# Kernel optimization log

Hardware: AMD Instinct MI355X
Metric: run time of the kernel (lower is better)

Reference implementation:

```python
import jax, jax.numpy as jnp
import numpy as np
import math

D_MODEL = 256
SIGMA = 1.0


def _sinusoidal_pe(L, d_model, dtype=jnp.float32):
    # pe[l, 2i] = sin(l * w_i), pe[l, 2i+1] = cos(l * w_i)
    position = jnp.arange(L, dtype=dtype)[:, None]                       # [L,1]
    div_term = jnp.exp(jnp.arange(0, d_model, 2, dtype=dtype) * (-math.log(10000.0) / d_model))
    pe = jnp.zeros((L, d_model), dtype=dtype)
    pe = pe.at[:, 0::2].set(jnp.sin(position * div_term))
    pe = pe.at[:, 1::2].set(jnp.cos(position * div_term))
    return pe  # [L, d_model]


def setup_inputs() -> dict:
    key = jax.random.key(0)
    # scale 0.05 keeps pairwise sq-distances O(1) so S = exp(-d/2) is non-degenerate
    x = jax.random.normal(key, (4, 4096, 256), dtype=jnp.float32) * 0.05
    return {"x": x}


def reference(x):
    B, L, D = x.shape
    pe = _sinusoidal_pe(L, D_MODEL, dtype=x.dtype)[None]                 # [1,L,D]
    # pairwise squared distances via the expansion ||a||^2+||b||^2-2ab (avoids [B,L,L,D])
    sq = jnp.sum(x * x, axis=-1)                                         # [B,L]
    gram = jnp.einsum('bld,bmd->blm', x, x)                              # [B,L,L]
    dist_sq = jnp.maximum(sq[:, :, None] + sq[:, None, :] - 2.0 * gram, 0.0)
    S = jnp.exp(-dist_sq / (2.0 * SIGMA ** 2))                           # [B,L,L]
    sem = jnp.einsum('blm,bmd->bld', S, x) / jnp.sum(S, axis=-1, keepdims=True)
    return x + pe + sem
```

## Files before the change

kernel.cpp:

```cpp
#include <hip/hip_runtime.h>

typedef unsigned char u8;
typedef float f32x4 __attribute__((ext_vector_type(4)));
typedef float f32x16 __attribute__((ext_vector_type(16)));
typedef int i32x8 __attribute__((ext_vector_type(8)));

#define LL 4096
#define PSTR 144
#define SCALE 16.0f
#define GSCALE (1.0f/256.0f)
#define FREQC (-0.03597789207803197f)
#define ONE_SC 0x7F7F7F7F
#define VBSTR 1048576l

__device__ __forceinline__ i32x8 PK16(uint4 a, uint4 b) {
  i32x8 r;
  r[0] = (int)a.x; r[1] = (int)a.y; r[2] = (int)a.z; r[3] = (int)a.w;
  r[4] = (int)b.x; r[5] = (int)b.y; r[6] = (int)b.z; r[7] = (int)b.w;
  return r;
}

typedef __attribute__((address_space(3))) u8 lds_u8;
typedef __attribute__((address_space(1))) u8 glb_u8;
__device__ __forceinline__ void dma16(const u8* g, u8* l) {
  __builtin_amdgcn_global_load_lds((const glb_u8*)g, (lds_u8*)l, 16, 0, 0);
}

__global__ __launch_bounds__(512) void prep4(const float* __restrict__ x, u8* __restrict__ xbf,
                                             u8* __restrict__ xT, float* __restrict__ sq) {
  __shared__ u8 T2[256 * 80];
  const int blk = blockIdx.x;
  const int b = blk >> 6, ch = blk & 63;
  const int j0 = ch << 6;
  const int tid = threadIdx.x;
  const int wv = tid >> 6, ln = tid & 63;
  const long bL = (long)b * LL;
  const float4* x4 = (const float4*)x + (bL + j0) * 64;
  unsigned* xb4 = (unsigned*)xbf + (bL + j0) * 64;

  #pragma unroll
  for (int g = 0; g < 2; ++g) {
    int pkw[4];
    #pragma unroll
    for (int ii = 0; ii < 4; ++ii) {
      const int row = 8 * wv + 4 * g + ii;
      float4 v = x4[row * 64 + ln];
      float s = v.x * v.x + v.y * v.y + v.z * v.z + v.w * v.w;
      #pragma unroll
      for (int o = 32; o; o >>= 1) s += __shfl_xor(s, o);
      if (ln == 0) sq[bL + j0 + row] = s;
      int pk = __builtin_amdgcn_cvt_pk_fp8_f32(v.x * SCALE, v.y * SCALE, 0, false);
      pk = __builtin_amdgcn_cvt_pk_fp8_f32(v.z * SCALE, v.w * SCALE, pk, true);
      const int sdw = ((((ln >> 2) ^ ((j0 + row) & 15)) << 2)) | (ln & 3);
      xb4[row * 64 + sdw] = (unsigned)pk;
      pkw[ii] = pk;
    }
    const int rb = 8 * wv + 4 * g;
    #pragma unroll
    for (int k = 0; k < 4; ++k) {
      const unsigned sel = (unsigned)(k | ((4 + k) << 8));
      unsigned m01 = __builtin_amdgcn_perm((unsigned)pkw[1], (unsigned)pkw[0], sel);
      unsigned m23 = __builtin_amdgcn_perm((unsigned)pkw[3], (unsigned)pkw[2], sel);
      unsigned tw  = __builtin_amdgcn_perm(m23, m01, 0x05040100u);
      *(unsigned*)(T2 + (4 * ln + k) * 80 + rb) = tw;
    }
  }
  __syncthreads();
  #pragma unroll
  for (int db = 0; db < 2; ++db) {
    const int d = db * 128 + (tid >> 2);
    const int cl = tid & 3;
    const int c16 = ((ch & 1) << 2) | cl;
    const int p = c16 ^ (d & 7);
    uint4 ov = *(const uint4*)(T2 + d * 80 + 16 * cl);
    *(uint4*)(xT + (long)b * VBSTR + (ch >> 1) * 32768 + d * 128 + (p << 4)) = ov;
  }
}

__global__ __launch_bounds__(512, 2) void tpe_main(
    const u8* __restrict__ xbf, const u8* __restrict__ xT,
    const float* __restrict__ sqv,
    const float* __restrict__ x, float* __restrict__ out) {
  __shared__ __align__(16) u8 Kt[2][32768];
  __shared__ __align__(16) u8 Vt[2][32768];
  __shared__ __align__(16) u8 Ps[2][64 * PSTR];
  __shared__ float lred[8][64];
  __shared__ float linv[64];

  const int tid = threadIdx.x;
  const int w = tid >> 6;
  const int lane = tid & 63;
  const int l15 = lane & 15, l31 = lane & 31;
  const int q4 = lane >> 4;
  const int q2 = lane >> 5;

  const int blk = blockIdx.x;
  const int b = (blk & 7) >> 1;
  const int qt = ((blk >> 3) << 1) | (blk & 1);
  const int q0 = qt << 6;
  const long bL = (long)b * LL;

  i32x8 qmx[4][2];
  float qa[4];
  #pragma unroll
  for (int t = 0; t < 4; ++t) {
    const int row = q0 + 16 * t + l15;
    const u8* qrow = xbf + ((bL + row) << 8);
    #pragma unroll
    for (int u = 0; u < 2; ++u) {
      const int cb = 8 * u + 2 * q4;
      uint4 lo = *(const uint4*)(qrow + (((cb + 0) ^ l15) << 4));
      uint4 hi = *(const uint4*)(qrow + (((cb + 1) ^ l15) << 4));
      qmx[t][u] = PK16(lo, hi);
    }
    qa[t] = -0.5f * sqv[bL + row];
  }

  f32x16 oacc[2];
  #pragma unroll
  for (int rb = 0; rb < 2; ++rb)
    #pragma unroll
    for (int k = 0; k < 16; ++k) oacc[rb][k] = 0.f;
  float rsacc[4] = {0.f, 0.f, 0.f, 0.f};

  const u8* kbat = xbf + (bL << 8);
  const u8* vbat = xT + (long)b * VBSTR;
  const int vrow = (32 * w + l31) << 7;
  const int vk7 = l31 & 7;

  i32x8 vfA[2], vfB[2];

  #pragma unroll
  for (int c = 0; c < 4; ++c) {
    int off = c * 8192 + tid * 16;
    dma16(kbat + off, Kt[0] + off);
    dma16(vbat + off, Vt[0] + off);
  }
  __syncthreads();

#define TPE_ITER(IT, KCUR, KNXT, VCUR, VNXT, PPREV, PCUR, VFC, VFN)                         \
  {                                                                                         \
    const int j0 = (IT) << 7;                                                               \
    if ((IT) < 31) {  \
      const u8* ks = kbat + ((long)((IT) + 1) << 15);                                       \
      const u8* vs = vbat + ((long)((IT) + 1) << 15);                                       \
      _Pragma("unroll")                                                                     \
      for (int c = 0; c < 4; ++c) {                                                         \
        int off = c * 8192 + tid * 16;                                                      \
        dma16(ks + off, (KNXT) + off);                                                      \
        dma16(vs + off, (VNXT) + off);                                                      \
      }                                                                                     \
    }                                                                                       \
    float4 skv4 = *(const float4*)(sqv + bL + j0 + 16 * w + 4 * q4);                        \
    if ((IT) != 0) {  \
      _Pragma("unroll")                                                                     \
      for (int u = 0; u < 2; ++u) {                                                         \
        const u8* pr0 = (PPREV) + l31 * PSTR + 64 * u + 32 * q2;                            \
        i32x8 pa0 = PK16(*(const uint4*)(pr0), *(const uint4*)(pr0 + 16));                  \
        i32x8 pa1 = PK16(*(const uint4*)(pr0 + 32 * PSTR),                                  \
                         *(const uint4*)(pr0 + 32 * PSTR + 16));                            \
        oacc[0] = __builtin_amdgcn_mfma_scale_f32_32x32x64_f8f6f4(                          \
            pa0, VFC[u], oacc[0], 0, 0, 0, ONE_SC, 0, ONE_SC);                              \
        oacc[1] = __builtin_amdgcn_mfma_scale_f32_32x32x64_f8f6f4(                          \
            pa1, VFC[u], oacc[1], 0, 0, 0, ONE_SC, 0, ONE_SC);                              \
      }                                                                                     \
    }                                                                                       \
    _Pragma("unroll")           \
    for (int u = 0; u < 2; ++u) {                                                           \
      const int cb = 4 * u + 2 * q2;                                                        \
      uint4 v0 = *(const uint4*)((VCUR) + vrow + (((cb + 0) ^ vk7) << 4));                  \
      uint4 v1 = *(const uint4*)((VCUR) + vrow + (((cb + 1) ^ vk7) << 4));                  \
      VFN[u] = PK16(v0, v1);                                                                \
    }                                                                                       \
    {                            \
      const int krow = 16 * w + l15;                                                        \
      const u8* kb2 = (KCUR) + krow * 256;                                                  \
      f32x4 sacc[4];                                                                        \
      _Pragma("unroll")                                                                     \
      for (int t = 0; t < 4; ++t) {                                                         \
        sacc[t][0] = 0.f; sacc[t][1] = 0.f; sacc[t][2] = 0.f; sacc[t][3] = 0.f;             \
      }                                                                                     \
      _Pragma("unroll")                                                                     \
      for (int u = 0; u < 2; ++u) {                                                         \
        const int cb = 8 * u + 2 * q4;                                                      \
        uint4 klo = *(const uint4*)(kb2 + (((cb + 0) ^ l15) << 4));                         \
        uint4 khi = *(const uint4*)(kb2 + (((cb + 1) ^ l15) << 4));                         \
        i32x8 af = PK16(klo, khi);                                                          \
        _Pragma("unroll")                                                                   \
        for (int t = 0; t < 4; ++t)                                                         \
          sacc[t] = __builtin_amdgcn_mfma_scale_f32_16x16x128_f8f6f4(                       \
              af, qmx[t][u], sacc[t], 0, 0, 0, ONE_SC, 0, ONE_SC);                          \
      }                                                                                     \
      _Pragma("unroll")        \
      for (int t = 0; t < 4; ++t) {                 \
        float p0 = __expf(fminf(fmaf(sacc[t][0], GSCALE, qa[t] + skv4.x), 0.f));            \
        float p1 = __expf(fminf(fmaf(sacc[t][1], GSCALE, qa[t] + skv4.y), 0.f));            \
        float p2 = __expf(fminf(fmaf(sacc[t][2], GSCALE, qa[t] + skv4.z), 0.f));            \
        float p3 = __expf(fminf(fmaf(sacc[t][3], GSCALE, qa[t] + skv4.w), 0.f));            \
        rsacc[t] += (p0 + p1) + (p2 + p3);                                                  \
        int pk = __builtin_amdgcn_cvt_pk_fp8_f32(p0, p1, 0, false);                         \
        pk = __builtin_amdgcn_cvt_pk_fp8_f32(p2, p3, pk, true);                             \
        *(int*)((PCUR) + (16 * t + l15) * PSTR + 16 * w + 4 * q4) = pk;                     \
      }                                                                                     \
    }                                                                                       \
    __syncthreads();                \
  }

  for (int it2 = 0; it2 < 16; ++it2) {
    TPE_ITER(2 * it2,     Kt[0], Kt[1], Vt[0], Vt[1], Ps[1], Ps[0], vfA, vfB)
    TPE_ITER(2 * it2 + 1, Kt[1], Kt[0], Vt[1], Vt[0], Ps[0], Ps[1], vfB, vfA)
  }
#undef TPE_ITER

  #pragma unroll
  for (int u = 0; u < 2; ++u) {
    const u8* pr0 = Ps[1] + l31 * PSTR + 64 * u + 32 * q2;
    i32x8 pa0 = PK16(*(const uint4*)(pr0), *(const uint4*)(pr0 + 16));
    i32x8 pa1 = PK16(*(const uint4*)(pr0 + 32 * PSTR), *(const uint4*)(pr0 + 32 * PSTR + 16));
    oacc[0] = __builtin_amdgcn_mfma_scale_f32_32x32x64_f8f6f4(
        pa0, vfA[u], oacc[0], 0, 0, 0, ONE_SC, 0, ONE_SC);
    oacc[1] = __builtin_amdgcn_mfma_scale_f32_32x32x64_f8f6f4(
        pa1, vfA[u], oacc[1], 0, 0, 0, ONE_SC, 0, ONE_SC);
  }

  #pragma unroll
  for (int t = 0; t < 4; ++t) {
    float r = rsacc[t];
    r += __shfl_xor(r, 16);
    r += __shfl_xor(r, 32);
    if (lane < 16) lred[w][16 * t + l15] = r;
  }
  __syncthreads();
  if (tid < 64) {
    float s = 0.f;
    #pragma unroll
    for (int ww = 0; ww < 8; ++ww) s += lred[ww][tid];
    linv[tid] = 0.0625f / s;
  }
  __syncthreads();
  const int col = 32 * w + l31;
  const float freq = __expf((float)(col & ~1) * FREQC);
  #pragma unroll
  for (int rb = 0; rb < 2; ++rb) {
    #pragma unroll
    for (int reg = 0; reg < 16; ++reg) {
      int row = 32 * rb + 4 * q2 + (reg & 3) + 8 * (reg >> 2);
      int l = q0 + row;
      float ang = (float)l * freq;
      float pv = (col & 1) ? __cosf(ang) : __sinf(ang);
      long off = ((bL + l) << 8) + col;
      out[off] = oacc[rb][reg] * linv[row] + x[off] + pv;
    }
  }
}

extern "C" void kernel_launch(void* const* d_in, const int* in_sizes, int n_in,
                              void* d_out, int out_size, void* d_ws, size_t ws_size,
                              hipStream_t stream) {
  const float* x = (const float*)d_in[0];
  float* out = (float*)d_out;
  char* ws = (char*)d_ws;
  u8* xbf = (u8*)ws;
  u8* xT = (u8*)(ws + 4194304);
  float* sq = (float*)(ws + 8388608);
  prep4<<<256, 512, 0, stream>>>(x, xbf, xT, sq);
  tpe_main<<<256, 512, 0, stream>>>(xbf, xT, sq, x, out);
}
```

Before: 123.7 us.

## Swizzle fp8 K/V at 32-byte granularity and fold log2e into exp2

Changes the XOR swizzle of the fp8 K (xbf) and transposed V (xT) buffers from 16-byte to 32-byte chunks, so each MFMA operand fragment becomes a single 32-byte LDS/global load instead of two 16-byte loads packed together. It also pre-multiplies the squared norms and gram scale by log2(e) so the Gaussian kernel uses exp2f directly. The aim is fewer LDS read instructions and a cheaper exponential. The coarser swizzle may raise LDS bank conflicts, and the new layout must match between the prep kernel and the main kernel.

Result: slower. 133.9 us (+8.3%).

```diff
diff --git a/kernel.cpp b/kernel.cpp
--- a/kernel.cpp
+++ b/kernel.cpp
@@ -9,6 +9,8 @@
 #define PSTR 144
 #define SCALE 16.0f
 #define GSCALE (1.0f/256.0f)
+#define L2E 1.44269504f
+#define GS2 (1.44269504f/256.0f)
 #define FREQC (-0.03597789207803197f)
 #define ONE_SC 0x7F7F7F7F
 #define VBSTR 1048576l
@@ -26,7 +28,7 @@
   __builtin_amdgcn_global_load_lds((const glb_u8*)g, (lds_u8*)l, 16, 0, 0);
 }
 
-__global__ __launch_bounds__(512) void prep4(const float* __restrict__ x, u8* __restrict__ xbf,
+__global__ __launch_bounds__(512) void prep5(const float* __restrict__ x, u8* __restrict__ xbf,
                                              u8* __restrict__ xT, float* __restrict__ sq) {
   __shared__ u8 T2[256 * 80];
   const int blk = blockIdx.x;
@@ -51,7 +53,7 @@
       if (ln == 0) sq[bL + j0 + row] = s;
       int pk = __builtin_amdgcn_cvt_pk_fp8_f32(v.x * SCALE, v.y * SCALE, 0, false);
       pk = __builtin_amdgcn_cvt_pk_fp8_f32(v.z * SCALE, v.w * SCALE, pk, true);
-      const int sdw = ((((ln >> 2) ^ ((j0 + row) & 15)) << 2)) | (ln & 3);
+      const int sdw = ((((ln >> 3) ^ ((j0 + row) & 7)) << 3)) | (ln & 7);
       xb4[row * 64 + sdw] = (unsigned)pk;
       pkw[ii] = pk;
     }
@@ -70,10 +72,10 @@
   for (int db = 0; db < 2; ++db) {
     const int d = db * 128 + (tid >> 2);
     const int cl = tid & 3;
-    const int c16 = ((ch & 1) << 2) | cl;
-    const int p = c16 ^ (d & 7);
+    const int c32 = ((ch & 1) << 1) | (cl >> 1);
+    const int p = c32 ^ (d & 3);
     uint4 ov = *(const uint4*)(T2 + d * 80 + 16 * cl);
-    *(uint4*)(xT + (long)b * VBSTR + (ch >> 1) * 32768 + d * 128 + (p << 4)) = ov;
+    *(uint4*)(xT + (long)b * VBSTR + (ch >> 1) * 32768 + d * 128 + (p << 5) + ((cl & 1) << 4)) = ov;
   }
 }
 
@@ -81,8 +83,8 @@
     const u8* __restrict__ xbf, const u8* __restrict__ xT,
     const float* __restrict__ sqv,
     const float* __restrict__ x, float* __restrict__ out) {
-  __shared__ __align__(16) u8 Kt[2][32768];
-  __shared__ __align__(16) u8 Vt[2][32768];
+  __shared__ __align__(32) u8 Kt[2][32768];
+  __shared__ __align__(32) u8 Vt[2][32768];
   __shared__ __align__(16) u8 Ps[2][64 * PSTR];
   __shared__ float lred[8][64];
   __shared__ float linv[64];
@@ -93,6 +95,8 @@
   const int l15 = lane & 15, l31 = lane & 31;
   const int q4 = lane >> 4;
   const int q2 = lane >> 5;
+  const int k7 = l15 & 7;
+  const int vk3 = l31 & 3;
 
   const int blk = blockIdx.x;
   const int b = (blk & 7) >> 1;
@@ -107,13 +111,9 @@
     const int row = q0 + 16 * t + l15;
     const u8* qrow = xbf + ((bL + row) << 8);
     #pragma unroll
-    for (int u = 0; u < 2; ++u) {
-      const int cb = 8 * u + 2 * q4;
-      uint4 lo = *(const uint4*)(qrow + (((cb + 0) ^ l15) << 4));
-      uint4 hi = *(const uint4*)(qrow + (((cb + 1) ^ l15) << 4));
-      qmx[t][u] = PK16(lo, hi);
-    }
-    qa[t] = -0.5f * sqv[bL + row];
+    for (int u = 0; u < 2; ++u)
+      qmx[t][u] = *(const i32x8*)(qrow + (((4 * u + q4) ^ k7) << 5));
+    qa[t] = (-0.5f * L2E) * sqv[bL + row];
   }
 
   f32x16 oacc[2];
@@ -126,7 +126,6 @@
   const u8* kbat = xbf + (bL << 8);
   const u8* vbat = xT + (long)b * VBSTR;
   const int vrow = (32 * w + l31) << 7;
-  const int vk7 = l31 & 7;
 
   i32x8 vfA[2], vfB[2];
 
@@ -152,6 +151,7 @@
       }                                                                                     \
     }                                                                                       \
     float4 skv4 = *(const float4*)(sqv + bL + j0 + 16 * w + 4 * q4);                        \
+    skv4.x *= L2E; skv4.y *= L2E; skv4.z *= L2E; skv4.w *= L2E;                             \
     if ((IT) != 0) {  \
       _Pragma("unroll")                                                                     \
       for (int u = 0; u < 2; ++u) {                                                         \
@@ -165,13 +165,9 @@
             pa1, VFC[u], oacc[1], 0, 0, 0, ONE_SC, 0, ONE_SC);                              \
       }                                                                                     \
     }                                                                                       \
-    _Pragma("unroll")           \
-    for (int u = 0; u < 2; ++u) {                                                           \
-      const int cb = 4 * u + 2 * q2;                                                        \
-      uint4 v0 = *(const uint4*)((VCUR) + vrow + (((cb + 0) ^ vk7) << 4));                  \
-      uint4 v1 = *(const uint4*)((VCUR) + vrow + (((cb + 1) ^ vk7) << 4));                  \
-      VFN[u] = PK16(v0, v1);                                                                \
-    }                                                                                       \
+    _Pragma("unroll")  \
+    for (int u = 0; u < 2; ++u)                                                             \
+      VFN[u] = *(const i32x8*)((VCUR) + vrow + (((2 * u + q2) ^ vk3) << 5));                \
     {                            \
       const int krow = 16 * w + l15;                                                        \
       const u8* kb2 = (KCUR) + krow * 256;                                                  \
@@ -182,21 +178,18 @@
       }                                                                                     \
       _Pragma("unroll")                                                                     \
       for (int u = 0; u < 2; ++u) {                                                         \
-        const int cb = 8 * u + 2 * q4;                                                      \
-        uint4 klo = *(const uint4*)(kb2 + (((cb + 0) ^ l15) << 4));                         \
-        uint4 khi = *(const uint4*)(kb2 + (((cb + 1) ^ l15) << 4));                         \
-        i32x8 af = PK16(klo, khi);                                                          \
+        i32x8 af = *(const i32x8*)(kb2 + (((4 * u + q4) ^ k7) << 5));                       \
         _Pragma("unroll")                                                                   \
         for (int t = 0; t < 4; ++t)                                                         \
           sacc[t] = __builtin_amdgcn_mfma_scale_f32_16x16x128_f8f6f4(                       \
               af, qmx[t][u], sacc[t], 0, 0, 0, ONE_SC, 0, ONE_SC);                          \
       }                                                                                     \
-      _Pragma("unroll")        \
+      _Pragma("unroll")     \
       for (int t = 0; t < 4; ++t) {                 \
-        float p0 = __expf(fminf(fmaf(sacc[t][0], GSCALE, qa[t] + skv4.x), 0.f));            \
-        float p1 = __expf(fminf(fmaf(sacc[t][1], GSCALE, qa[t] + skv4.y), 0.f));            \
-        float p2 = __expf(fminf(fmaf(sacc[t][2], GSCALE, qa[t] + skv4.z), 0.f));            \
-        float p3 = __expf(fminf(fmaf(sacc[t][3], GSCALE, qa[t] + skv4.w), 0.f));            \
+        float p0 = exp2f(fminf(fmaf(sacc[t][0], GS2, qa[t] + skv4.x), 0.f));                \
+        float p1 = exp2f(fminf(fmaf(sacc[t][1], GS2, qa[t] + skv4.y), 0.f));                \
+        float p2 = exp2f(fminf(fmaf(sacc[t][2], GS2, qa[t] + skv4.z), 0.f));                \
+        float p3 = exp2f(fminf(fmaf(sacc[t][3], GS2, qa[t] + skv4.w), 0.f));                \
         rsacc[t] += (p0 + p1) + (p2 + p3);                                                  \
         int pk = __builtin_amdgcn_cvt_pk_fp8_f32(p0, p1, 0, false);                         \
         pk = __builtin_amdgcn_cvt_pk_fp8_f32(p2, p3, pk, true);                             \
@@ -263,6 +256,6 @@
   u8* xbf = (u8*)ws;
   u8* xT = (u8*)(ws + 4194304);
   float* sq = (float*)(ws + 8388608);
-  prep4<<<256, 512, 0, stream>>>(x, xbf, xT, sq);
+  prep5<<<256, 512, 0, stream>>>(x, xbf, xT, sq);
   tpe_main<<<256, 512, 0, stream>>>(xbf, xT, sq, x, out);
 }
```

## Pad V tile rows to 136 bytes, shrink P stride, use exp2 scaling

Applied to the files above, without the earlier changes.

Pads each transposed-V row in global memory and LDS from 128 to 136 bytes, and shrinks the P staging stride from 144 to 136. The goal is to change LDS bank mapping and cut bank conflicts on the V-fragment and P-fragment reads. Because the padded rows are no longer 16-byte aligned, those reads become 8-byte loads. The change also folds log2(e) into the query and key norm terms so the kernel can call exp2f in place of __expf. The padded layout needs more workspace, so a fallback path keeps the original 128-byte layout when the workspace is too small.

After: 132.7 us. 1.07x slower.

```diff
diff --git a/kernel.cpp b/kernel.cpp
--- a/kernel.cpp
+++ b/kernel.cpp
@@ -6,12 +6,12 @@
 typedef int i32x8 __attribute__((ext_vector_type(8)));
 
 #define LL 4096
-#define PSTR 144
+#define PSTR 136
 #define SCALE 16.0f
-#define GSCALE (1.0f/256.0f)
+#define L2E 1.44269504f
+#define GS2 (1.44269504f/256.0f)
 #define FREQC (-0.03597789207803197f)
 #define ONE_SC 0x7F7F7F7F
-#define VBSTR 1048576l
 
 __device__ __forceinline__ i32x8 PK16(uint4 a, uint4 b) {
   i32x8 r;
@@ -19,6 +19,12 @@
   r[4] = (int)b.x; r[5] = (int)b.y; r[6] = (int)b.z; r[7] = (int)b.w;
   return r;
 }
+__device__ __forceinline__ i32x8 PK8(uint2 a, uint2 b, uint2 c, uint2 d) {
+  i32x8 r;
+  r[0] = (int)a.x; r[1] = (int)a.y; r[2] = (int)b.x; r[3] = (int)b.y;
+  r[4] = (int)c.x; r[5] = (int)c.y; r[6] = (int)d.x; r[7] = (int)d.y;
+  return r;
+}
 
 typedef __attribute__((address_space(3))) u8 lds_u8;
 typedef __attribute__((address_space(1))) u8 glb_u8;
@@ -26,8 +32,9 @@
   __builtin_amdgcn_global_load_lds((const glb_u8*)g, (lds_u8*)l, 16, 0, 0);
 }
 
-__global__ __launch_bounds__(512) void prep4(const float* __restrict__ x, u8* __restrict__ xbf,
-                                             u8* __restrict__ xT, float* __restrict__ sq) {
+template<int VROW>
+__global__ __launch_bounds__(512) void prep_t(const float* __restrict__ x, u8* __restrict__ xbf,
+                                              u8* __restrict__ xT, float* __restrict__ sq) {
   __shared__ u8 T2[256 * 80];
   const int blk = blockIdx.x;
   const int b = blk >> 6, ch = blk & 63;
@@ -73,16 +80,25 @@
     const int c16 = ((ch & 1) << 2) | cl;
     const int p = c16 ^ (d & 7);
     uint4 ov = *(const uint4*)(T2 + d * 80 + 16 * cl);
-    *(uint4*)(xT + (long)b * VBSTR + (ch >> 1) * 32768 + d * 128 + (p << 4)) = ov;
-  }
-}
-
-__global__ __launch_bounds__(512, 2) void tpe_main(
+    u8* dst = xT + (long)b * (32l * 256 * VROW) + (ch >> 1) * (256 * VROW) + d * VROW + (p << 4);
+    if constexpr ((VROW & 15) != 0) {
+      uint2 lo; lo.x = ov.x; lo.y = ov.y;
+      uint2 hi; hi.x = ov.z; hi.y = ov.w;
+      *(uint2*)dst = lo;
+      *(uint2*)(dst + 8) = hi;
+    } else {
+      *(uint4*)dst = ov;
+    }
+  }
+}
+
+template<int VROW>
+__global__ __launch_bounds__(512, 2) void tpe_main_t(
     const u8* __restrict__ xbf, const u8* __restrict__ xT,
     const float* __restrict__ sqv,
     const float* __restrict__ x, float* __restrict__ out) {
   __shared__ __align__(16) u8 Kt[2][32768];
-  __shared__ __align__(16) u8 Vt[2][32768];
+  __shared__ __align__(16) u8 Vt[2][256 * VROW];
   __shared__ __align__(16) u8 Ps[2][64 * PSTR];
   __shared__ float lred[8][64];
   __shared__ float linv[64];
@@ -113,7 +129,7 @@
       uint4 hi = *(const uint4*)(qrow + (((cb + 1) ^ l15) << 4));
       qmx[t][u] = PK16(lo, hi);
     }
-    qa[t] = -0.5f * sqv[bL + row];
+    qa[t] = (-0.5f * L2E) * sqv[bL + row];
   }
 
   f32x16 oacc[2];
@@ -124,9 +140,10 @@
   float rsacc[4] = {0.f, 0.f, 0.f, 0.f};
 
   const u8* kbat = xbf + (bL << 8);
-  const u8* vbat = xT + (long)b * VBSTR;
-  const int vrow = (32 * w + l31) << 7;
+  const u8* vbat = xT + (long)b * (32l * 256 * VROW);
+  const int vrowB = (32 * w + l31) * VROW;
   const int vk7 = l31 & 7;
+  constexpr int VBYTES = 256 * VROW;
 
   i32x8 vfA[2], vfB[2];
 
@@ -136,41 +153,55 @@
     dma16(kbat + off, Kt[0] + off);
     dma16(vbat + off, Vt[0] + off);
   }
+  if constexpr (VBYTES > 32768) {
+    if (tid * 16 < VBYTES - 32768) dma16(vbat + 32768 + tid * 16, Vt[0] + 32768 + tid * 16);
+  }
   __syncthreads();
 
 #define TPE_ITER(IT, KCUR, KNXT, VCUR, VNXT, PPREV, PCUR, VFC, VFN)                         \
   {                                                                                         \
-    const int j0 = (IT) << 7;                                                               \
     if ((IT) < 31) {  \
       const u8* ks = kbat + ((long)((IT) + 1) << 15);                                       \
-      const u8* vs = vbat + ((long)((IT) + 1) << 15);                                       \
+      const u8* vs = vbat + (long)((IT) + 1) * VBYTES;                                      \
       _Pragma("unroll")                                                                     \
       for (int c = 0; c < 4; ++c) {                                                         \
         int off = c * 8192 + tid * 16;                                                      \
         dma16(ks + off, (KNXT) + off);                                                      \
         dma16(vs + off, (VNXT) + off);                                                      \
       }                                                                                     \
+      if constexpr (VBYTES > 32768) {                                                       \
+        if (tid * 16 < VBYTES - 32768)                                                      \
+          dma16(vs + 32768 + tid * 16, (VNXT) + 32768 + tid * 16);                          \
+      }                                                                                     \
     }                                                                                       \
-    float4 skv4 = *(const float4*)(sqv + bL + j0 + 16 * w + 4 * q4);                        \
-    if ((IT) != 0) {  \
+    float4 skv4 = *(const float4*)(sqv + bL + ((IT) << 7) + 16 * w + 4 * q4);               \
+    skv4.x *= L2E; skv4.y *= L2E; skv4.z *= L2E; skv4.w *= L2E;                             \
+    if ((IT) != 0) {   \
       _Pragma("unroll")                                                                     \
       for (int u = 0; u < 2; ++u) {                                                         \
         const u8* pr0 = (PPREV) + l31 * PSTR + 64 * u + 32 * q2;                            \
-        i32x8 pa0 = PK16(*(const uint4*)(pr0), *(const uint4*)(pr0 + 16));                  \
-        i32x8 pa1 = PK16(*(const uint4*)(pr0 + 32 * PSTR),                                  \
-                         *(const uint4*)(pr0 + 32 * PSTR + 16));                            \
+        const u8* pr1 = pr0 + 32 * PSTR;                                                    \
+        i32x8 pa0 = PK8(*(const uint2*)(pr0),      *(const uint2*)(pr0 + 8),                \
+                        *(const uint2*)(pr0 + 16), *(const uint2*)(pr0 + 24));              \
+        i32x8 pa1 = PK8(*(const uint2*)(pr1),      *(const uint2*)(pr1 + 8),                \
+                        *(const uint2*)(pr1 + 16), *(const uint2*)(pr1 + 24));              \
         oacc[0] = __builtin_amdgcn_mfma_scale_f32_32x32x64_f8f6f4(                          \
             pa0, VFC[u], oacc[0], 0, 0, 0, ONE_SC, 0, ONE_SC);                              \
         oacc[1] = __builtin_amdgcn_mfma_scale_f32_32x32x64_f8f6f4(                          \
             pa1, VFC[u], oacc[1], 0, 0, 0, ONE_SC, 0, ONE_SC);                              \
       }                                                                                     \
     }                                                                                       \
-    _Pragma("unroll")           \
+    _Pragma("unroll")               \
     for (int u = 0; u < 2; ++u) {                                                           \
       const int cb = 4 * u + 2 * q2;                                                        \
-      uint4 v0 = *(const uint4*)((VCUR) + vrow + (((cb + 0) ^ vk7) << 4));                  \
-      uint4 v1 = *(const uint4*)((VCUR) + vrow + (((cb + 1) ^ vk7) << 4));                  \
-      VFN[u] = PK16(v0, v1);                                                                \
+      const u8* v0p = (VCUR) + vrowB + (((cb + 0) ^ vk7) << 4);                             \
+      const u8* v1p = (VCUR) + vrowB + (((cb + 1) ^ vk7) << 4);                             \
+      if constexpr ((VROW & 15) != 0) {                   \
+        VFN[u] = PK8(*(const uint2*)v0p, *(const uint2*)(v0p + 8),                          \
+                     *(const uint2*)v1p, *(const uint2*)(v1p + 8));                         \
+      } else {                                       \
+        VFN[u] = PK16(*(const uint4*)v0p, *(const uint4*)v1p);                              \
+      }                                                                                     \
     }                                                                                       \
     {                            \
       const int krow = 16 * w + l15;                                                        \
@@ -191,12 +222,12 @@
           sacc[t] = __builtin_amdgcn_mfma_scale_f32_16x16x128_f8f6f4(                       \
               af, qmx[t][u], sacc[t], 0, 0, 0, ONE_SC, 0, ONE_SC);                          \
       }                                                                                     \
-      _Pragma("unroll")        \
+      _Pragma("unroll")                     \
       for (int t = 0; t < 4; ++t) {                 \
-        float p0 = __expf(fminf(fmaf(sacc[t][0], GSCALE, qa[t] + skv4.x), 0.f));            \
-        float p1 = __expf(fminf(fmaf(sacc[t][1], GSCALE, qa[t] + skv4.y), 0.f));            \
-        float p2 = __expf(fminf(fmaf(sacc[t][2], GSCALE, qa[t] + skv4.z), 0.f));            \
-        float p3 = __expf(fminf(fmaf(sacc[t][3], GSCALE, qa[t] + skv4.w), 0.f));            \
+        float p0 = exp2f(fminf(fmaf(sacc[t][0], GS2, qa[t] + skv4.x), 0.f));                \
+        float p1 = exp2f(fminf(fmaf(sacc[t][1], GS2, qa[t] + skv4.y), 0.f));                \
+        float p2 = exp2f(fminf(fmaf(sacc[t][2], GS2, qa[t] + skv4.z), 0.f));                \
+        float p3 = exp2f(fminf(fmaf(sacc[t][3], GS2, qa[t] + skv4.w), 0.f));                \
         rsacc[t] += (p0 + p1) + (p2 + p3);                                                  \
         int pk = __builtin_amdgcn_cvt_pk_fp8_f32(p0, p1, 0, false);                         \
         pk = __builtin_amdgcn_cvt_pk_fp8_f32(p2, p3, pk, true);                             \
@@ -215,8 +246,11 @@
   #pragma unroll
   for (int u = 0; u < 2; ++u) {
     const u8* pr0 = Ps[1] + l31 * PSTR + 64 * u + 32 * q2;
-    i32x8 pa0 = PK16(*(const uint4*)(pr0), *(const uint4*)(pr0 + 16));
-    i32x8 pa1 = PK16(*(const uint4*)(pr0 + 32 * PSTR), *(const uint4*)(pr0 + 32 * PSTR + 16));
+    const u8* pr1 = pr0 + 32 * PSTR;
+    i32x8 pa0 = PK8(*(const uint2*)(pr0),      *(const uint2*)(pr0 + 8),
+                    *(const uint2*)(pr0 + 16), *(const uint2*)(pr0 + 24));
+    i32x8 pa1 = PK8(*(const uint2*)(pr1),      *(const uint2*)(pr1 + 8),
+                    *(const uint2*)(pr1 + 16), *(const uint2*)(pr1 + 24));
     oacc[0] = __builtin_amdgcn_mfma_scale_f32_32x32x64_f8f6f4(
         pa0, vfA[u], oacc[0], 0, 0, 0, ONE_SC, 0, ONE_SC);
     oacc[1] = __builtin_amdgcn_mfma_scale_f32_32x32x64_f8f6f4(
@@ -262,7 +296,14 @@
   char* ws = (char*)d_ws;
   u8* xbf = (u8*)ws;
   u8* xT = (u8*)(ws + 4194304);
-  float* sq = (float*)(ws + 8388608);
-  prep4<<<256, 512, 0, stream>>>(x, xbf, xT, sq);
-  tpe_main<<<256, 512, 0, stream>>>(xbf, xT, sq, x, out);
-}
+  const size_t need136 = 4194304ul + 4456448ul + 65536ul;
+  if (ws_size >= need136) {
+    float* sq = (float*)(ws + 4194304 + 4456448);
+    prep_t<136><<<256, 512, 0, stream>>>(x, xbf, xT, sq);
+    tpe_main_t<136><<<256, 512, 0, stream>>>(xbf, xT, sq, x, out);
+  } else {
+    float* sq = (float*)(ws + 8388608);
+    prep_t<128><<<256, 512, 0, stream>>>(x, xbf, xT, sq);
+    tpe_main_t<128><<<256, 512, 0, stream>>>(xbf, xT, sq, x, out);
+  }
+}
```

## Split block into producer waves for QK/exp and consumer waves for PV

Applied to the files above, without the earlier changes.

Warp-specializes the attention kernel: waves 0-3 load K tiles, compute QK^T scores and exp probabilities into LDS, while waves 4-7 load V tiles and run the P·V MFMAs one tile behind. Each group now does twice the per-wave work of its own stage, with the two halves matched by shared __syncthreads calls. The aim is to overlap the exp/VALU-heavy stage with the MFMA-heavy stage across waves. The cost is a pipeline built on counted barriers in divergent branches, which is fragile, and consumers hold four 32x32 accumulators, raising register pressure.

New measurement: 125.6 us. No clear change (+1.6%).

```diff
diff --git a/kernel.cpp b/kernel.cpp
--- a/kernel.cpp
+++ b/kernel.cpp
@@ -84,7 +84,7 @@
   __shared__ __align__(16) u8 Kt[2][32768];
   __shared__ __align__(16) u8 Vt[2][32768];
   __shared__ __align__(16) u8 Ps[2][64 * PSTR];
-  __shared__ float lred[8][64];
+  __shared__ float lred[4][64];
   __shared__ float linv[64];
 
   const int tid = threadIdx.x;
@@ -100,35 +100,8 @@
   const int q0 = qt << 6;
   const long bL = (long)b * LL;
 
-  i32x8 qmx[4][2];
-  float qa[4];
-  #pragma unroll
-  for (int t = 0; t < 4; ++t) {
-    const int row = q0 + 16 * t + l15;
-    const u8* qrow = xbf + ((bL + row) << 8);
-    #pragma unroll
-    for (int u = 0; u < 2; ++u) {
-      const int cb = 8 * u + 2 * q4;
-      uint4 lo = *(const uint4*)(qrow + (((cb + 0) ^ l15) << 4));
-      uint4 hi = *(const uint4*)(qrow + (((cb + 1) ^ l15) << 4));
-      qmx[t][u] = PK16(lo, hi);
-    }
-    qa[t] = -0.5f * sqv[bL + row];
-  }
-
-  f32x16 oacc[2];
-  #pragma unroll
-  for (int rb = 0; rb < 2; ++rb)
-    #pragma unroll
-    for (int k = 0; k < 16; ++k) oacc[rb][k] = 0.f;
-  float rsacc[4] = {0.f, 0.f, 0.f, 0.f};
-
   const u8* kbat = xbf + (bL << 8);
   const u8* vbat = xT + (long)b * VBSTR;
-  const int vrow = (32 * w + l31) << 7;
-  const int vk7 = l31 & 7;
-
-  i32x8 vfA[2], vfB[2];
 
   #pragma unroll
   for (int c = 0; c < 4; ++c) {
@@ -138,43 +111,40 @@
   }
   __syncthreads();
 
-#define TPE_ITER(IT, KCUR, KNXT, VCUR, VNXT, PPREV, PCUR, VFC, VFN)                         \
+  if (w < 4) {
+    i32x8 qmx[4][2];
+    float qa[4];
+    float rsacc[4] = {0.f, 0.f, 0.f, 0.f};
+    #pragma unroll
+    for (int t = 0; t < 4; ++t) {
+      const int row = q0 + 16 * t + l15;
+      const u8* qrow = xbf + ((bL + row) << 8);
+      #pragma unroll
+      for (int u = 0; u < 2; ++u) {
+        const int cb = 8 * u + 2 * q4;
+        uint4 lo = *(const uint4*)(qrow + (((cb + 0) ^ l15) << 4));
+        uint4 hi = *(const uint4*)(qrow + (((cb + 1) ^ l15) << 4));
+        qmx[t][u] = PK16(lo, hi);
+      }
+      qa[t] = -0.5f * sqv[bL + row];
+    }
+
+#define PROD_ITER(IT, KCUR, KNXT, PCUR)                                                     \
   {                                                                                         \
     const int j0 = (IT) << 7;                                                               \
-    if ((IT) < 31) {  \
+    if ((IT) < 31) {          \
       const u8* ks = kbat + ((long)((IT) + 1) << 15);                                       \
-      const u8* vs = vbat + ((long)((IT) + 1) << 15);                                       \
-      _Pragma("unroll")                                                                     \
-      for (int c = 0; c < 4; ++c) {                                                         \
-        int off = c * 8192 + tid * 16;                                                      \
+      _Pragma("unroll")                                                                     \
+      for (int c = 0; c < 8; ++c) {                                                         \
+        int off = c * 4096 + tid * 16;                                                      \
         dma16(ks + off, (KNXT) + off);                                                      \
-        dma16(vs + off, (VNXT) + off);                                                      \
-      }                                                                                     \
-    }                                                                                       \
-    float4 skv4 = *(const float4*)(sqv + bL + j0 + 16 * w + 4 * q4);                        \
-    if ((IT) != 0) {  \
-      _Pragma("unroll")                                                                     \
-      for (int u = 0; u < 2; ++u) {                                                         \
-        const u8* pr0 = (PPREV) + l31 * PSTR + 64 * u + 32 * q2;                            \
-        i32x8 pa0 = PK16(*(const uint4*)(pr0), *(const uint4*)(pr0 + 16));                  \
-        i32x8 pa1 = PK16(*(const uint4*)(pr0 + 32 * PSTR),                                  \
-                         *(const uint4*)(pr0 + 32 * PSTR + 16));                            \
-        oacc[0] = __builtin_amdgcn_mfma_scale_f32_32x32x64_f8f6f4(                          \
-            pa0, VFC[u], oacc[0], 0, 0, 0, ONE_SC, 0, ONE_SC);                              \
-        oacc[1] = __builtin_amdgcn_mfma_scale_f32_32x32x64_f8f6f4(                          \
-            pa1, VFC[u], oacc[1], 0, 0, 0, ONE_SC, 0, ONE_SC);                              \
-      }                                                                                     \
-    }                                                                                       \
-    _Pragma("unroll")           \
-    for (int u = 0; u < 2; ++u) {                                                           \
-      const int cb = 4 * u + 2 * q2;                                                        \
-      uint4 v0 = *(const uint4*)((VCUR) + vrow + (((cb + 0) ^ vk7) << 4));                  \
-      uint4 v1 = *(const uint4*)((VCUR) + vrow + (((cb + 1) ^ vk7) << 4));                  \
-      VFN[u] = PK16(v0, v1);                                                                \
-    }                                                                                       \
-    {                            \
-      const int krow = 16 * w + l15;                                                        \
-      const u8* kb2 = (KCUR) + krow * 256;                                                  \
+      }                                                                                     \
+    }                                                                                       \
+    _Pragma("unroll")                                                                       \
+    for (int s = 0; s < 2; ++s) {                              \
+      const int wj = 2 * w + s;                                                             \
+      float4 skv4 = *(const float4*)(sqv + bL + j0 + 16 * wj + 4 * q4);                     \
+      const u8* kb2 = (KCUR) + (16 * wj + l15) * 256;                                       \
       f32x4 sacc[4];                                                                        \
       _Pragma("unroll")                                                                     \
       for (int t = 0; t < 4; ++t) {                                                         \
@@ -191,8 +161,8 @@
           sacc[t] = __builtin_amdgcn_mfma_scale_f32_16x16x128_f8f6f4(                       \
               af, qmx[t][u], sacc[t], 0, 0, 0, ONE_SC, 0, ONE_SC);                          \
       }                                                                                     \
-      _Pragma("unroll")        \
-      for (int t = 0; t < 4; ++t) {                 \
+      _Pragma("unroll")                                                                     \
+      for (int t = 0; t < 4; ++t) {                \
         float p0 = __expf(fminf(fmaf(sacc[t][0], GSCALE, qa[t] + skv4.x), 0.f));            \
         float p1 = __expf(fminf(fmaf(sacc[t][1], GSCALE, qa[t] + skv4.y), 0.f));            \
         float p2 = __expf(fminf(fmaf(sacc[t][2], GSCALE, qa[t] + skv4.z), 0.f));            \
@@ -200,56 +170,113 @@
         rsacc[t] += (p0 + p1) + (p2 + p3);                                                  \
         int pk = __builtin_amdgcn_cvt_pk_fp8_f32(p0, p1, 0, false);                         \
         pk = __builtin_amdgcn_cvt_pk_fp8_f32(p2, p3, pk, true);                             \
-        *(int*)((PCUR) + (16 * t + l15) * PSTR + 16 * w + 4 * q4) = pk;                     \
-      }                                                                                     \
-    }                                                                                       \
-    __syncthreads();                \
-  }
-
-  for (int it2 = 0; it2 < 16; ++it2) {
-    TPE_ITER(2 * it2,     Kt[0], Kt[1], Vt[0], Vt[1], Ps[1], Ps[0], vfA, vfB)
-    TPE_ITER(2 * it2 + 1, Kt[1], Kt[0], Vt[1], Vt[0], Ps[0], Ps[1], vfB, vfA)
-  }
-#undef TPE_ITER
-
-  #pragma unroll
-  for (int u = 0; u < 2; ++u) {
-    const u8* pr0 = Ps[1] + l31 * PSTR + 64 * u + 32 * q2;
-    i32x8 pa0 = PK16(*(const uint4*)(pr0), *(const uint4*)(pr0 + 16));
-    i32x8 pa1 = PK16(*(const uint4*)(pr0 + 32 * PSTR), *(const uint4*)(pr0 + 32 * PSTR + 16));
-    oacc[0] = __builtin_amdgcn_mfma_scale_f32_32x32x64_f8f6f4(
-        pa0, vfA[u], oacc[0], 0, 0, 0, ONE_SC, 0, ONE_SC);
-    oacc[1] = __builtin_amdgcn_mfma_scale_f32_32x32x64_f8f6f4(
-        pa1, vfA[u], oacc[1], 0, 0, 0, ONE_SC, 0, ONE_SC);
-  }
-
-  #pragma unroll
-  for (int t = 0; t < 4; ++t) {
-    float r = rsacc[t];
-    r += __shfl_xor(r, 16);
-    r += __shfl_xor(r, 32);
-    if (lane < 16) lred[w][16 * t + l15] = r;
-  }
-  __syncthreads();
-  if (tid < 64) {
-    float s = 0.f;
-    #pragma unroll
-    for (int ww = 0; ww < 8; ++ww) s += lred[ww][tid];
-    linv[tid] = 0.0625f / s;
-  }
-  __syncthreads();
-  const int col = 32 * w + l31;
-  const float freq = __expf((float)(col & ~1) * FREQC);
-  #pragma unroll
-  for (int rb = 0; rb < 2; ++rb) {
-    #pragma unroll
-    for (int reg = 0; reg < 16; ++reg) {
-      int row = 32 * rb + 4 * q2 + (reg & 3) + 8 * (reg >> 2);
-      int l = q0 + row;
-      float ang = (float)l * freq;
-      float pv = (col & 1) ? __cosf(ang) : __sinf(ang);
-      long off = ((bL + l) << 8) + col;
-      out[off] = oacc[rb][reg] * linv[row] + x[off] + pv;
+        *(int*)((PCUR) + (16 * t + l15) * PSTR + 16 * wj + 4 * q4) = pk;                    \
+      }                                                                                     \
+    }                                                                                       \
+    __syncthreads();                                                                        \
+  }
+
+    for (int it2 = 0; it2 < 16; ++it2) {
+      PROD_ITER(2 * it2,     Kt[0], Kt[1], Ps[0])
+      PROD_ITER(2 * it2 + 1, Kt[1], Kt[0], Ps[1])
+    }
+#undef PROD_ITER
+
+    #pragma unroll
+    for (int t = 0; t < 4; ++t) {
+      float r = rsacc[t];
+      r += __shfl_xor(r, 16);
+      r += __shfl_xor(r, 32);
+      if (lane < 16) lred[w][16 * t + l15] = r;
+    }
+    __syncthreads();
+    if (tid < 64) {
+      float sfull = 0.f;
+      #pragma unroll
+      for (int ww = 0; ww < 4; ++ww) sfull += lred[ww][tid];
+      linv[tid] = 0.0625f / sfull;
+    }
+    __syncthreads();
+  } else {
+    const int wc = w - 4;
+    const int ctid = tid - 256;
+    const int vk7 = l31 & 7;
+    const int vrow0 = ((64 * wc + l31) << 7);
+    const int vrow1 = vrow0 + (32 << 7);
+    f32x16 oacc[4];
+    #pragma unroll
+    for (int k = 0; k < 4; ++k)
+      #pragma unroll
+      for (int kk = 0; kk < 16; ++kk) oacc[k][kk] = 0.f;
+
+#define CONS_MM2(PSRC, VSRC)                                                                \
+  {                                                                                         \
+    _Pragma("unroll")                                                                       \
+    for (int u = 0; u < 2; ++u) {                                                           \
+      const u8* pr0 = (PSRC) + l31 * PSTR + 64 * u + 32 * q2;                               \
+      i32x8 pa0 = PK16(*(const uint4*)(pr0), *(const uint4*)(pr0 + 16));                    \
+      i32x8 pa1 = PK16(*(const uint4*)(pr0 + 32 * PSTR),                                    \
+                       *(const uint4*)(pr0 + 32 * PSTR + 16));                              \
+      const int cb = 4 * u + 2 * q2;                                                        \
+      uint4 v00 = *(const uint4*)((VSRC) + vrow0 + (((cb + 0) ^ vk7) << 4));                \
+      uint4 v01 = *(const uint4*)((VSRC) + vrow0 + (((cb + 1) ^ vk7) << 4));                \
+      uint4 v10 = *(const uint4*)((VSRC) + vrow1 + (((cb + 0) ^ vk7) << 4));                \
+      uint4 v11 = *(const uint4*)((VSRC) + vrow1 + (((cb + 1) ^ vk7) << 4));                \
+      i32x8 vf0 = PK16(v00, v01);                                                           \
+      i32x8 vf1 = PK16(v10, v11);                                                           \
+      oacc[0] = __builtin_amdgcn_mfma_scale_f32_32x32x64_f8f6f4(                            \
+          pa0, vf0, oacc[0], 0, 0, 0, ONE_SC, 0, ONE_SC);                                   \
+      oacc[1] = __builtin_amdgcn_mfma_scale_f32_32x32x64_f8f6f4(                            \
+          pa1, vf0, oacc[1], 0, 0, 0, ONE_SC, 0, ONE_SC);                                   \
+      oacc[2] = __builtin_amdgcn_mfma_scale_f32_32x32x64_f8f6f4(                            \
+          pa0, vf1, oacc[2], 0, 0, 0, ONE_SC, 0, ONE_SC);                                   \
+      oacc[3] = __builtin_amdgcn_mfma_scale_f32_32x32x64_f8f6f4(                            \
+          pa1, vf1, oacc[3], 0, 0, 0, ONE_SC, 0, ONE_SC);                                   \
+    }                                                                                       \
+  }
+
+#define CONS_ITER(IT, PPREV, VPREV, VNXT)                                                   \
+  {                                                                                         \
+    if ((IT) != 0) CONS_MM2(PPREV, VPREV)           \
+    if ((IT) < 31) {          \
+      const u8* vs = vbat + ((long)((IT) + 1) << 15);                                       \
+      _Pragma("unroll")                                                                     \
+      for (int c = 0; c < 8; ++c) {                                                         \
+        int off = c * 4096 + ctid * 16;                                                     \
+        dma16(vs + off, (VNXT) + off);                                                      \
+      }                                                                                     \
+    }                                                                                       \
+    __syncthreads();                                                                        \
+  }
+
+    for (int it2 = 0; it2 < 16; ++it2) {
+      CONS_ITER(2 * it2,     Ps[1], Vt[1], Vt[1])
+      CONS_ITER(2 * it2 + 1, Ps[0], Vt[0], Vt[0])
+    }
+#undef CONS_ITER
+
+    CONS_MM2(Ps[1], Vt[1])
+#undef CONS_MM2
+
+    __syncthreads();
+    __syncthreads();
+
+    #pragma unroll
+    for (int db = 0; db < 2; ++db) {
+      const int col = 64 * wc + 32 * db + l31;
+      const float freq = __expf((float)(col & ~1) * FREQC);
+      #pragma unroll
+      for (int rb = 0; rb < 2; ++rb) {
+        #pragma unroll
+        for (int reg = 0; reg < 16; ++reg) {
+          int row = 32 * rb + 4 * q2 + (reg & 3) + 8 * (reg >> 2);
+          int l = q0 + row;
+          float ang = (float)l * freq;
+          float pv = (col & 1) ? __cosf(ang) : __sinf(ang);
+          long off = ((bL + l) << 8) + col;
+          out[off] = oacc[2 * db + rb][reg] * linv[row] + x[off] + pv;
+        }
+      }
     }
   }
 }
```
